# Kernel optimization log

Measured on AMD Instinct MI355X. Metric: run time of the kernel, lower is better.

The kernel has to match this reference:

```python
import jax, jax.numpy as jnp
import numpy as np

TOKENS = 8192       # batch 4 * seq 2048
D_IN = 4096
D_OUT = 4096


def setup_inputs() -> dict:
    key = jax.random.key(0)
    k_x, k_w, k_s, k_b = jax.random.split(key, 4)
    x = jax.random.normal(k_x, (TOKENS, D_IN), dtype=jnp.float32)
    # symmetric int8 quantized weight rows in [-128, 127]
    weight_q = jax.random.randint(k_w, (D_OUT, D_IN), -128, 128, dtype=jnp.int32)
    # per-output-channel scales (positive, small, like max_abs / 127)
    scales = jax.random.uniform(k_s, (D_OUT,), dtype=jnp.float32, minval=1e-4, maxval=2e-2)
    bias = jax.random.normal(k_b, (D_OUT,), dtype=jnp.float32)
    return {"x": x, "weight_q": weight_q, "scales": scales, "bias": bias}


def reference(x, weight_q, scales, bias):
    # Per-channel dequant: W[o, i] = weight_q[o, i] * scales[o]  (zero_point = 0)
    w = weight_q.astype(jnp.float32) * scales[:, None]          # [D_OUT, D_IN]
    # F.linear: x @ W^T + bias
    return jnp.einsum("ti,oi->to", x, w) + bias                 # [TOKENS, D_OUT]
```

## Files before the change

kernel.cpp:

```cpp
#include <hip/hip_runtime.h>
#include <stdint.h>

#define M_TOK 8192
#define N_OUT 4096
#define K_IN  4096

#define BM 256
#define BN 256
#define BK 128
#define NT (K_IN / BK)
#define NIT (NT / 2)

typedef __attribute__((ext_vector_type(4))) int i32x4;

__global__ void quant_x_kernel(const float* __restrict__ x,
                               char* __restrict__ A8,
                               float* __restrict__ sx) {
  int row = blockIdx.x * 4 + (threadIdx.x >> 6);
  int lane = threadIdx.x & 63;
  const float* xr = x + (size_t)row * K_IN;

  float4 v[4][4];
  float mx = 0.f;
#pragma unroll
  for (int c = 0; c < 4; ++c) {
    int base = c * 1024 + lane * 16;
#pragma unroll
    for (int j = 0; j < 4; ++j) {
      v[c][j] = *reinterpret_cast<const float4*>(xr + base + j * 4);
      mx = fmaxf(mx, fmaxf(fmaxf(fabsf(v[c][j].x), fabsf(v[c][j].y)),
                           fmaxf(fabsf(v[c][j].z), fabsf(v[c][j].w))));
    }
  }
#pragma unroll
  for (int m = 32; m > 0; m >>= 1) mx = fmaxf(mx, __shfl_xor(mx, m));

  float inv = (mx > 0.f) ? (127.0f / mx) : 0.f;
  if (lane == 0) sx[row] = (mx > 0.f) ? (mx / 127.0f) : 1.0f;

#pragma unroll
  for (int c = 0; c < 4; ++c) {
    int qi[16];
#pragma unroll
    for (int j = 0; j < 4; ++j) {
      qi[j * 4 + 0] = __float2int_rn(v[c][j].x * inv);
      qi[j * 4 + 1] = __float2int_rn(v[c][j].y * inv);
      qi[j * 4 + 2] = __float2int_rn(v[c][j].z * inv);
      qi[j * 4 + 3] = __float2int_rn(v[c][j].w * inv);
    }
    int4 p;
    int* pp = (int*)&p;
#pragma unroll
    for (int w = 0; w < 4; ++w) {
      int a0 = min(127, max(-127, qi[w * 4 + 0])) & 0xff;
      int a1 = min(127, max(-127, qi[w * 4 + 1])) & 0xff;
      int a2 = min(127, max(-127, qi[w * 4 + 2])) & 0xff;
      int a3 = min(127, max(-127, qi[w * 4 + 3])) & 0xff;
      pp[w] = a0 | (a1 << 8) | (a2 << 16) | (a3 << 24);
    }
    *reinterpret_cast<int4*>(A8 + (size_t)row * K_IN + c * 1024 + lane * 16) = p;
  }
}

__global__ void pack_w_kernel(const int* __restrict__ wq, char* __restrict__ B8) {
  const int total = (N_OUT * K_IN) / 16;
  for (int i = blockIdx.x * blockDim.x + threadIdx.x; i < total;
       i += gridDim.x * blockDim.x) {
    int4 p;
    int* pp = (int*)&p;
#pragma unroll
    for (int w = 0; w < 4; ++w) {
      int4 s = reinterpret_cast<const int4*>(wq)[i * 4 + w];
      pp[w] = (s.x & 0xff) | ((s.y & 0xff) << 8) | ((s.z & 0xff) << 16) |
              ((s.w & 0xff) << 24);
    }
    reinterpret_cast<int4*>(B8)[i] = p;
  }
}

#define GLOAD_LDS16(gptr, lptr)                                               \
  __builtin_amdgcn_global_load_lds(                                           \
      (const __attribute__((address_space(1))) void*)(gptr),                  \
      (__attribute__((address_space(3))) void*)(lptr), 16, 0, 0)

#define WAITCNT(s) asm volatile("s_waitcnt " s ::: "memory")

#define LDSA(buf, mh, fm, kk)                                                 \
  (*reinterpret_cast<const i32x4*>(                                           \
      lds + (buf)*65536 + (mh)*16384 + aRow + (fm)*2048 +                     \
      (((((kk)*4) | sBase) ^ sXor) << 4)))
#define LDSB(buf, nh, fn, kk)                                                 \
  (*reinterpret_cast<const i32x4*>(                                           \
      lds + (buf)*65536 + 32768 + (nh)*16384 + bRow + (fn)*2048 +             \
      (((((kk)*4) | sBase) ^ sXor) << 4)))

#define STAGE_A(buf, h, kt)                                                   \
  do {                                                                        \
    const char* _s = stA + (size_t)(h) * 128 * K_IN + (kt) * BK;              \
    GLOAD_LDS16(_s, lds + (buf)*65536 + (h)*16384 + ldsW0);                   \
    GLOAD_LDS16(_s + (size_t)64 * K_IN,                                       \
                lds + (buf)*65536 + (h)*16384 + 8192 + ldsW0);                \
  } while (0)
#define STAGE_B(buf, h, kt)                                                   \
  do {                                                                        \
    const char* _s = stB + (size_t)(h) * 128 * K_IN + (kt) * BK;              \
    GLOAD_LDS16(_s, lds + (buf)*65536 + 32768 + (h)*16384 + ldsW0);           \
    GLOAD_LDS16(_s + (size_t)64 * K_IN,                                       \
                lds + (buf)*65536 + 32768 + (h)*16384 + 8192 + ldsW0);        \
  } while (0)

#define MFMA16(mh, nh, BR)                                                    \
  do {                                                                        \
    _Pragma("unroll") for (int fm = 0; fm < 4; ++fm)                          \
    _Pragma("unroll") for (int fn = 0; fn < 2; ++fn) {                        \
      acc[mh][nh][fm][fn] = __builtin_amdgcn_mfma_i32_16x16x64_i8(            \
          aR[fm][0], BR[fn][0], acc[mh][nh][fm][fn], 0, 0, 0);                \
      acc[mh][nh][fm][fn] = __builtin_amdgcn_mfma_i32_16x16x64_i8(            \
          aR[fm][1], BR[fn][1], acc[mh][nh][fm][fn], 0, 0, 0);                \
    }                                                                         \
  } while (0)

#define PH_MID()                                                              \
  __builtin_amdgcn_s_barrier();                                               \
  WAITCNT("lgkmcnt(0)");                                                      \
  __builtin_amdgcn_sched_barrier(0);                                          \
  __builtin_amdgcn_s_setprio(1)

#define PH_END()                                                              \
  __builtin_amdgcn_s_setprio(0);                                              \
  __builtin_amdgcn_s_barrier();                                               \
  __builtin_amdgcn_sched_barrier(0)

#define PH_END_VM()                                                           \
  __builtin_amdgcn_s_setprio(0);                                              \
  WAITCNT("vmcnt(6)");                                                        \
  __builtin_amdgcn_sched_barrier(0);                                          \
  __builtin_amdgcn_s_barrier();                                               \
  __builtin_amdgcn_sched_barrier(0)

__global__ __launch_bounds__(512, 2) void gemm_8ph_i8(
    const char* __restrict__ A,
    const char* __restrict__ B,
    const float* __restrict__ sx,
    const float* __restrict__ scales,
    const float* __restrict__ bias,
    float* __restrict__ out) {
  __shared__ __align__(1024) char lds[131072];

  int bid = blockIdx.x;
  int swz = (bid & 7) * (512 / 8) + (bid >> 3);
  int bx = swz & 15;
  int by = swz >> 4;

  int tid = threadIdx.x;
  int lane = tid & 63;
  int wid = tid >> 6;
  int wm = wid >> 2;
  int wn = wid & 3;

  int aRow = (wm * 64 + (lane & 15)) * 128;
  int bRow = (wn * 32 + (lane & 15)) * 128;
  int sBase = lane >> 4;
  int sXor = lane & 7;

  const char* stA = A + (size_t)(by * BM + wid * 8 + (lane >> 3)) * K_IN +
                    ((lane & 7) ^ (lane >> 3)) * 16;
  const char* stB = B + (size_t)(bx * BN + wid * 8 + (lane >> 3)) * K_IN +
                    ((lane & 7) ^ (lane >> 3)) * 16;
  int ldsW0 = wid * 1024;

  i32x4 acc[2][2][4][2] = {};
  i32x4 aR[4][2];
  i32x4 bR0[2][2], bR1[2][2];

  STAGE_A(0, 0, 0); STAGE_A(0, 1, 0); STAGE_B(0, 0, 0); STAGE_B(0, 1, 0);
  WAITCNT("vmcnt(4)");
  STAGE_A(1, 0, 1); STAGE_B(1, 0, 1); STAGE_B(1, 1, 1);
  WAITCNT("vmcnt(6)");
  __builtin_amdgcn_s_barrier();
  __builtin_amdgcn_sched_barrier(0);

#pragma unroll 1
  for (int it = 0; it < NIT; ++it) {
    int kt1 = 2 * it + 1;
    int kt2 = (2 * it + 2) & (NT - 1);
    int kt3 = (2 * it + 3) & (NT - 1);

#pragma unroll
    for (int fm = 0; fm < 4; ++fm) { aR[fm][0] = LDSA(0, 0, fm, 0); aR[fm][1] = LDSA(0, 0, fm, 1); }
#pragma unroll
    for (int fn = 0; fn < 2; ++fn) { bR0[fn][0] = LDSB(0, 0, fn, 0); bR0[fn][1] = LDSB(0, 0, fn, 1); }
    STAGE_A(1, 1, kt1);
    WAITCNT("lgkmcnt(8)");
    PH_MID();
    MFMA16(0, 0, bR0);
    PH_END();

#pragma unroll
    for (int fn = 0; fn < 2; ++fn) { bR1[fn][0] = LDSB(0, 1, fn, 0); bR1[fn][1] = LDSB(0, 1, fn, 1); }
    STAGE_A(0, 0, kt2);
    PH_MID();
    MFMA16(0, 1, bR1);
    PH_END();

#pragma unroll
    for (int fm = 0; fm < 4; ++fm) { aR[fm][0] = LDSA(0, 1, fm, 0); aR[fm][1] = LDSA(0, 1, fm, 1); }
    STAGE_B(0, 0, kt2);
    PH_MID();
    MFMA16(1, 1, bR1);
    PH_END();

    STAGE_B(0, 1, kt2);
    PH_MID();
    MFMA16(1, 0, bR0);
    PH_END_VM();

#pragma unroll
    for (int fm = 0; fm < 4; ++fm) { aR[fm][0] = LDSA(1, 0, fm, 0); aR[fm][1] = LDSA(1, 0, fm, 1); }
#pragma unroll
    for (int fn = 0; fn < 2; ++fn) { bR0[fn][0] = LDSB(1, 0, fn, 0); bR0[fn][1] = LDSB(1, 0, fn, 1); }
    STAGE_A(0, 1, kt2);
    WAITCNT("lgkmcnt(8)");
    PH_MID();
    MFMA16(0, 0, bR0);
    PH_END();

#pragma unroll
    for (int fn = 0; fn < 2; ++fn) { bR1[fn][0] = LDSB(1, 1, fn, 0); bR1[fn][1] = LDSB(1, 1, fn, 1); }
    STAGE_A(1, 0, kt3);
    PH_MID();
    MFMA16(0, 1, bR1);
    PH_END();

#pragma unroll
    for (int fm = 0; fm < 4; ++fm) { aR[fm][0] = LDSA(1, 1, fm, 0); aR[fm][1] = LDSA(1, 1, fm, 1); }
    STAGE_B(1, 0, kt3);
    PH_MID();
    MFMA16(1, 1, bR1);
    PH_END();

    STAGE_B(1, 1, kt3);
    PH_MID();
    MFMA16(1, 0, bR0);
    PH_END_VM();
  }

  float sxv[2][4][4];
#pragma unroll
  for (int mh = 0; mh < 2; ++mh)
#pragma unroll
    for (int fm = 0; fm < 4; ++fm) {
      int row0 = by * BM + mh * 128 + wm * 64 + fm * 16 + (lane >> 4) * 4;
#pragma unroll
      for (int r = 0; r < 4; ++r) sxv[mh][fm][r] = sx[row0 + r];
    }

#pragma unroll
  for (int nh = 0; nh < 2; ++nh)
#pragma unroll
    for (int fn = 0; fn < 2; ++fn) {
      int col = bx * BN + nh * 128 + wn * 32 + fn * 16 + (lane & 15);
      float so = scales[col];
      float bv = bias[col];
#pragma unroll
      for (int mh = 0; mh < 2; ++mh)
#pragma unroll
        for (int fm = 0; fm < 4; ++fm) {
          int row0 = by * BM + mh * 128 + wm * 64 + fm * 16 + (lane >> 4) * 4;
          i32x4 v = acc[mh][nh][fm][fn];
#pragma unroll
          for (int r = 0; r < 4; ++r)
            out[(size_t)(row0 + r) * N_OUT + col] =
                (float)v[r] * (sxv[mh][fm][r] * so) + bv;
        }
    }
}

__global__ void fallback_gemm(const float* __restrict__ x,
                              const int* __restrict__ wq,
                              const float* __restrict__ scales,
                              const float* __restrict__ bias,
                              float* __restrict__ out) {
  __shared__ float xs[64][33];
  __shared__ float ws_[64][33];
  int tx = threadIdx.x & 15;
  int ty = threadIdx.x >> 4;
  int brow = blockIdx.y * 64, bcol = blockIdx.x * 64;
  float acc[4][4] = {};
  for (int k0 = 0; k0 < K_IN; k0 += 32) {
    for (int i = threadIdx.x; i < 64 * 32; i += 256) {
      int r = i >> 5, c = i & 31;
      xs[r][c] = x[(size_t)(brow + r) * K_IN + k0 + c];
      ws_[r][c] = (float)wq[(size_t)(bcol + r) * K_IN + k0 + c];
    }
    __syncthreads();
#pragma unroll 8
    for (int k = 0; k < 32; ++k) {
      float xv[4], wv[4];
#pragma unroll
      for (int i = 0; i < 4; ++i) xv[i] = xs[ty * 4 + i][k];
#pragma unroll
      for (int j = 0; j < 4; ++j) wv[j] = ws_[tx * 4 + j][k];
#pragma unroll
      for (int i = 0; i < 4; ++i)
#pragma unroll
        for (int j = 0; j < 4; ++j) acc[i][j] += xv[i] * wv[j];
    }
    __syncthreads();
  }
#pragma unroll
  for (int i = 0; i < 4; ++i)
#pragma unroll
    for (int j = 0; j < 4; ++j) {
      int o = bcol + tx * 4 + j;
      out[(size_t)(brow + ty * 4 + i) * N_OUT + o] = acc[i][j] * scales[o] + bias[o];
    }
}

extern "C" void kernel_launch(void* const* d_in, const int* in_sizes, int n_in,
                              void* d_out, int out_size, void* d_ws, size_t ws_size,
                              hipStream_t stream) {
  const float* x = (const float*)d_in[0];
  const int* wq = (const int*)d_in[1];
  const float* scales = (const float*)d_in[2];
  const float* bias = (const float*)d_in[3];
  float* out = (float*)d_out;

  const size_t offB = (size_t)M_TOK * K_IN;
  const size_t offS = offB + (size_t)N_OUT * K_IN;
  const size_t need = offS + (size_t)M_TOK * 4;

  if (ws_size >= need) {
    char* A8 = (char*)d_ws;
    char* B8 = (char*)d_ws + offB;
    float* sx = (float*)((char*)d_ws + offS);
    quant_x_kernel<<<M_TOK / 4, 256, 0, stream>>>(x, A8, sx);
    pack_w_kernel<<<2048, 256, 0, stream>>>(wq, B8);
    gemm_8ph_i8<<<(M_TOK / BM) * (N_OUT / BN), 512, 0, stream>>>(
        A8, B8, sx, scales, bias, out);
  } else {
    dim3 grid(N_OUT / 64, M_TOK / 64);
    fallback_gemm<<<grid, 256, 0, stream>>>(x, wq, scales, bias, out);
  }
}
```

Measured before the change: 187.6 us.

## Switch GEMM to 32x32x32 int8 MFMA and merge prep kernels into one launch

Replaces the 16x16x64 int8 MFMA tiling with 32x32x32 int8 MFMA, which changes the LDS fragment addressing, the accumulator layout (i32x16) and the epilogue row mapping. It also fuses the activation quantization and weight packing kernels into a single launch using block-index dispatch. The larger MFMA shape is meant to cut LDS read traffic per flop and the instruction count, and the merged prep removes one kernel launch. The trade-off is higher register pressure from the wider accumulators and a different per-instruction throughput profile.

New measurement: 198.0 us. 5.6% more time.

```diff
diff --git a/kernel.cpp b/kernel.cpp
--- a/kernel.cpp
+++ b/kernel.cpp
@@ -12,69 +12,72 @@
 #define NIT (NT / 2)
 
 typedef __attribute__((ext_vector_type(4))) int i32x4;
-
-__global__ void quant_x_kernel(const float* __restrict__ x,
-                               char* __restrict__ A8,
-                               float* __restrict__ sx) {
-  int row = blockIdx.x * 4 + (threadIdx.x >> 6);
-  int lane = threadIdx.x & 63;
-  const float* xr = x + (size_t)row * K_IN;
-
-  float4 v[4][4];
-  float mx = 0.f;
-#pragma unroll
-  for (int c = 0; c < 4; ++c) {
-    int base = c * 1024 + lane * 16;
-#pragma unroll
-    for (int j = 0; j < 4; ++j) {
-      v[c][j] = *reinterpret_cast<const float4*>(xr + base + j * 4);
-      mx = fmaxf(mx, fmaxf(fmaxf(fabsf(v[c][j].x), fabsf(v[c][j].y)),
-                           fmaxf(fabsf(v[c][j].z), fabsf(v[c][j].w))));
-    }
-  }
-#pragma unroll
-  for (int m = 32; m > 0; m >>= 1) mx = fmaxf(mx, __shfl_xor(mx, m));
-
-  float inv = (mx > 0.f) ? (127.0f / mx) : 0.f;
-  if (lane == 0) sx[row] = (mx > 0.f) ? (mx / 127.0f) : 1.0f;
-
-#pragma unroll
-  for (int c = 0; c < 4; ++c) {
-    int qi[16];
-#pragma unroll
-    for (int j = 0; j < 4; ++j) {
-      qi[j * 4 + 0] = __float2int_rn(v[c][j].x * inv);
-      qi[j * 4 + 1] = __float2int_rn(v[c][j].y * inv);
-      qi[j * 4 + 2] = __float2int_rn(v[c][j].z * inv);
-      qi[j * 4 + 3] = __float2int_rn(v[c][j].w * inv);
-    }
-    int4 p;
-    int* pp = (int*)&p;
-#pragma unroll
-    for (int w = 0; w < 4; ++w) {
-      int a0 = min(127, max(-127, qi[w * 4 + 0])) & 0xff;
-      int a1 = min(127, max(-127, qi[w * 4 + 1])) & 0xff;
-      int a2 = min(127, max(-127, qi[w * 4 + 2])) & 0xff;
-      int a3 = min(127, max(-127, qi[w * 4 + 3])) & 0xff;
-      pp[w] = a0 | (a1 << 8) | (a2 << 16) | (a3 << 24);
-    }
-    *reinterpret_cast<int4*>(A8 + (size_t)row * K_IN + c * 1024 + lane * 16) = p;
-  }
-}
-
-__global__ void pack_w_kernel(const int* __restrict__ wq, char* __restrict__ B8) {
-  const int total = (N_OUT * K_IN) / 16;
-  for (int i = blockIdx.x * blockDim.x + threadIdx.x; i < total;
-       i += gridDim.x * blockDim.x) {
-    int4 p;
-    int* pp = (int*)&p;
-#pragma unroll
-    for (int w = 0; w < 4; ++w) {
-      int4 s = reinterpret_cast<const int4*>(wq)[i * 4 + w];
-      pp[w] = (s.x & 0xff) | ((s.y & 0xff) << 8) | ((s.z & 0xff) << 16) |
-              ((s.w & 0xff) << 24);
-    }
-    reinterpret_cast<int4*>(B8)[i] = p;
+typedef __attribute__((ext_vector_type(16))) int i32x16;
+
+__global__ void prep_kernel(const float* __restrict__ x,
+                            const int* __restrict__ wq,
+                            char* __restrict__ A8,
+                            float* __restrict__ sx,
+                            char* __restrict__ B8) {
+  if (blockIdx.x < M_TOK / 4) {
+    int row = blockIdx.x * 4 + (threadIdx.x >> 6);
+    int lane = threadIdx.x & 63;
+    const float* xr = x + (size_t)row * K_IN;
+
+    float4 v[4][4];
+    float mx = 0.f;
+#pragma unroll
+    for (int c = 0; c < 4; ++c) {
+      int base = c * 1024 + lane * 16;
+#pragma unroll
+      for (int j = 0; j < 4; ++j) {
+        v[c][j] = *reinterpret_cast<const float4*>(xr + base + j * 4);
+        mx = fmaxf(mx, fmaxf(fmaxf(fabsf(v[c][j].x), fabsf(v[c][j].y)),
+                             fmaxf(fabsf(v[c][j].z), fabsf(v[c][j].w))));
+      }
+    }
+#pragma unroll
+    for (int m = 32; m > 0; m >>= 1) mx = fmaxf(mx, __shfl_xor(mx, m));
+
+    float inv = (mx > 0.f) ? (127.0f / mx) : 0.f;
+    if (lane == 0) sx[row] = (mx > 0.f) ? (mx / 127.0f) : 1.0f;
+
+#pragma unroll
+    for (int c = 0; c < 4; ++c) {
+      int qi[16];
+#pragma unroll
+      for (int j = 0; j < 4; ++j) {
+        qi[j * 4 + 0] = __float2int_rn(v[c][j].x * inv);
+        qi[j * 4 + 1] = __float2int_rn(v[c][j].y * inv);
+        qi[j * 4 + 2] = __float2int_rn(v[c][j].z * inv);
+        qi[j * 4 + 3] = __float2int_rn(v[c][j].w * inv);
+      }
+      int4 p;
+      int* pp = (int*)&p;
+#pragma unroll
+      for (int w = 0; w < 4; ++w) {
+        int a0 = min(127, max(-127, qi[w * 4 + 0])) & 0xff;
+        int a1 = min(127, max(-127, qi[w * 4 + 1])) & 0xff;
+        int a2 = min(127, max(-127, qi[w * 4 + 2])) & 0xff;
+        int a3 = min(127, max(-127, qi[w * 4 + 3])) & 0xff;
+        pp[w] = a0 | (a1 << 8) | (a2 << 16) | (a3 << 24);
+      }
+      *reinterpret_cast<int4*>(A8 + (size_t)row * K_IN + c * 1024 + lane * 16) = p;
+    }
+  } else {
+    const int total = (N_OUT * K_IN) / 16;
+    int idx = (blockIdx.x - M_TOK / 4) * blockDim.x + threadIdx.x;
+    for (int i = idx; i < total; i += 1024 * 256) {
+      int4 p;
+      int* pp = (int*)&p;
+#pragma unroll
+      for (int w = 0; w < 4; ++w) {
+        int4 s = reinterpret_cast<const int4*>(wq)[i * 4 + w];
+        pp[w] = (s.x & 0xff) | ((s.y & 0xff) << 8) | ((s.z & 0xff) << 16) |
+                ((s.w & 0xff) << 24);
+      }
+      reinterpret_cast<int4*>(B8)[i] = p;
+    }
   }
 }
 
@@ -85,14 +88,14 @@
 
 #define WAITCNT(s) asm volatile("s_waitcnt " s ::: "memory")
 
-#define LDSA(buf, mh, fm, kk)                                                 \
+#define LDSA32(buf, mh, t, ks)                                                \
   (*reinterpret_cast<const i32x4*>(                                           \
-      lds + (buf)*65536 + (mh)*16384 + aRow + (fm)*2048 +                     \
-      (((((kk)*4) | sBase) ^ sXor) << 4)))
-#define LDSB(buf, nh, fn, kk)                                                 \
+      lds + (buf)*65536 + (mh)*16384 + (t)*4096 + aRowB +                     \
+      (((((ks)*2) | sHi) ^ sXor) << 4)))
+#define LDSB32(buf, nh, ks)                                                   \
   (*reinterpret_cast<const i32x4*>(                                           \
-      lds + (buf)*65536 + 32768 + (nh)*16384 + bRow + (fn)*2048 +             \
-      (((((kk)*4) | sBase) ^ sXor) << 4)))
+      lds + (buf)*65536 + 32768 + (nh)*16384 + bRowB +                        \
+      (((((ks)*2) | sHi) ^ sXor) << 4)))
 
 #define STAGE_A(buf, h, kt)                                                   \
   do {                                                                        \
@@ -109,15 +112,12 @@
                 lds + (buf)*65536 + 32768 + (h)*16384 + 8192 + ldsW0);        \
   } while (0)
 
-#define MFMA16(mh, nh, BR)                                                    \
+#define MFMA8(mh, nh, BR)                                                     \
   do {                                                                        \
-    _Pragma("unroll") for (int fm = 0; fm < 4; ++fm)                          \
-    _Pragma("unroll") for (int fn = 0; fn < 2; ++fn) {                        \
-      acc[mh][nh][fm][fn] = __builtin_amdgcn_mfma_i32_16x16x64_i8(            \
-          aR[fm][0], BR[fn][0], acc[mh][nh][fm][fn], 0, 0, 0);                \
-      acc[mh][nh][fm][fn] = __builtin_amdgcn_mfma_i32_16x16x64_i8(            \
-          aR[fm][1], BR[fn][1], acc[mh][nh][fm][fn], 0, 0, 0);                \
-    }                                                                         \
+    _Pragma("unroll") for (int ks = 0; ks < 4; ++ks)                          \
+    _Pragma("unroll") for (int t = 0; t < 2; ++t)                             \
+      acc[2 * (mh) + t][nh] = __builtin_amdgcn_mfma_i32_32x32x32_i8(          \
+          aR[t][ks], BR[ks], acc[2 * (mh) + t][nh], 0, 0, 0);                 \
   } while (0)
 
 #define PH_MID()                                                              \
@@ -138,7 +138,7 @@
   __builtin_amdgcn_s_barrier();                                               \
   __builtin_amdgcn_sched_barrier(0)
 
-__global__ __launch_bounds__(512, 2) void gemm_8ph_i8(
+__global__ __launch_bounds__(512, 2) void gemm_8ph_i8w(
     const char* __restrict__ A,
     const char* __restrict__ B,
     const float* __restrict__ sx,
@@ -158,9 +158,9 @@
   int wm = wid >> 2;
   int wn = wid & 3;
 
-  int aRow = (wm * 64 + (lane & 15)) * 128;
-  int bRow = (wn * 32 + (lane & 15)) * 128;
-  int sBase = lane >> 4;
+  int aRowB = (wm * 64 + (lane & 31)) * 128;
+  int bRowB = (wn * 32 + (lane & 31)) * 128;
+  int sHi = lane >> 5;
   int sXor = lane & 7;
 
   const char* stA = A + (size_t)(by * BM + wid * 8 + (lane >> 3)) * K_IN +
@@ -169,9 +169,9 @@
                     ((lane & 7) ^ (lane >> 3)) * 16;
   int ldsW0 = wid * 1024;
 
-  i32x4 acc[2][2][4][2] = {};
-  i32x4 aR[4][2];
-  i32x4 bR0[2][2], bR1[2][2];
+  i32x16 acc[4][2] = {};
+  i32x4 aR[2][4];
+  i32x4 bR0[4], bR1[4];
 
   STAGE_A(0, 0, 0); STAGE_A(0, 1, 0); STAGE_B(0, 0, 0); STAGE_B(0, 1, 0);
   WAITCNT("vmcnt(4)");
@@ -187,93 +187,93 @@
     int kt3 = (2 * it + 3) & (NT - 1);
 
 #pragma unroll
-    for (int fm = 0; fm < 4; ++fm) { aR[fm][0] = LDSA(0, 0, fm, 0); aR[fm][1] = LDSA(0, 0, fm, 1); }
-#pragma unroll
-    for (int fn = 0; fn < 2; ++fn) { bR0[fn][0] = LDSB(0, 0, fn, 0); bR0[fn][1] = LDSB(0, 0, fn, 1); }
+    for (int t = 0; t < 2; ++t)
+#pragma unroll
+      for (int ks = 0; ks < 4; ++ks) aR[t][ks] = LDSA32(0, 0, t, ks);
+#pragma unroll
+    for (int ks = 0; ks < 4; ++ks) bR0[ks] = LDSB32(0, 0, ks);
     STAGE_A(1, 1, kt1);
     WAITCNT("lgkmcnt(8)");
     PH_MID();
-    MFMA16(0, 0, bR0);
-    PH_END();
-
-#pragma unroll
-    for (int fn = 0; fn < 2; ++fn) { bR1[fn][0] = LDSB(0, 1, fn, 0); bR1[fn][1] = LDSB(0, 1, fn, 1); }
+    MFMA8(0, 0, bR0);
+    PH_END();
+
+#pragma unroll
+    for (int ks = 0; ks < 4; ++ks) bR1[ks] = LDSB32(0, 1, ks);
     STAGE_A(0, 0, kt2);
     PH_MID();
-    MFMA16(0, 1, bR1);
-    PH_END();
-
-#pragma unroll
-    for (int fm = 0; fm < 4; ++fm) { aR[fm][0] = LDSA(0, 1, fm, 0); aR[fm][1] = LDSA(0, 1, fm, 1); }
+    MFMA8(0, 1, bR1);
+    PH_END();
+
+#pragma unroll
+    for (int t = 0; t < 2; ++t)
+#pragma unroll
+      for (int ks = 0; ks < 4; ++ks) aR[t][ks] = LDSA32(0, 1, t, ks);
     STAGE_B(0, 0, kt2);
     PH_MID();
-    MFMA16(1, 1, bR1);
+    MFMA8(1, 1, bR1);
     PH_END();
 
     STAGE_B(0, 1, kt2);
     PH_MID();
-    MFMA16(1, 0, bR0);
+    MFMA8(1, 0, bR0);
     PH_END_VM();
 
 #pragma unroll
-    for (int fm = 0; fm < 4; ++fm) { aR[fm][0] = LDSA(1, 0, fm, 0); aR[fm][1] = LDSA(1, 0, fm, 1); }
-#pragma unroll
-    for (int fn = 0; fn < 2; ++fn) { bR0[fn][0] = LDSB(1, 0, fn, 0); bR0[fn][1] = LDSB(1, 0, fn, 1); }
+    for (int t = 0; t < 2; ++t)
+#pragma unroll
+      for (int ks = 0; ks < 4; ++ks) aR[t][ks] = LDSA32(1, 0, t, ks);
+#pragma unroll
+    for (int ks = 0; ks < 4; ++ks) bR0[ks] = LDSB32(1, 0, ks);
     STAGE_A(0, 1, kt2);
     WAITCNT("lgkmcnt(8)");
     PH_MID();
-    MFMA16(0, 0, bR0);
-    PH_END();
-
-#pragma unroll
-    for (int fn = 0; fn < 2; ++fn) { bR1[fn][0] = LDSB(1, 1, fn, 0); bR1[fn][1] = LDSB(1, 1, fn, 1); }
+    MFMA8(0, 0, bR0);
+    PH_END();
+
+#pragma unroll
+    for (int ks = 0; ks < 4; ++ks) bR1[ks] = LDSB32(1, 1, ks);
     STAGE_A(1, 0, kt3);
     PH_MID();
-    MFMA16(0, 1, bR1);
-    PH_END();
-
-#pragma unroll
-    for (int fm = 0; fm < 4; ++fm) { aR[fm][0] = LDSA(1, 1, fm, 0); aR[fm][1] = LDSA(1, 1, fm, 1); }
+    MFMA8(0, 1, bR1);
+    PH_END();
+
+#pragma unroll
+    for (int t = 0; t < 2; ++t)
+#pragma unroll
+      for (int ks = 0; ks < 4; ++ks) aR[t][ks] = LDSA32(1, 1, t, ks);
     STAGE_B(1, 0, kt3);
     PH_MID();
-    MFMA16(1, 1, bR1);
+    MFMA8(1, 1, bR1);
     PH_END();
 
     STAGE_B(1, 1, kt3);
     PH_MID();
-    MFMA16(1, 0, bR0);
+    MFMA8(1, 0, bR0);
     PH_END_VM();
   }
 
-  float sxv[2][4][4];
-#pragma unroll
-  for (int mh = 0; mh < 2; ++mh)
-#pragma unroll
-    for (int fm = 0; fm < 4; ++fm) {
-      int row0 = by * BM + mh * 128 + wm * 64 + fm * 16 + (lane >> 4) * 4;
-#pragma unroll
-      for (int r = 0; r < 4; ++r) sxv[mh][fm][r] = sx[row0 + r];
-    }
-
-#pragma unroll
-  for (int nh = 0; nh < 2; ++nh)
-#pragma unroll
-    for (int fn = 0; fn < 2; ++fn) {
-      int col = bx * BN + nh * 128 + wn * 32 + fn * 16 + (lane & 15);
+#pragma unroll
+  for (int tm = 0; tm < 4; ++tm) {
+    int mh = tm >> 1, t = tm & 1;
+    int rbase = by * BM + mh * 128 + wm * 64 + t * 32 + 4 * sHi;
+    float sxr[16];
+#pragma unroll
+    for (int reg = 0; reg < 16; ++reg)
+      sxr[reg] = sx[rbase + (reg & 3) + 8 * (reg >> 2)];
+#pragma unroll
+    for (int nh = 0; nh < 2; ++nh) {
+      int col = bx * BN + nh * 128 + wn * 32 + (lane & 31);
       float so = scales[col];
       float bv = bias[col];
-#pragma unroll
-      for (int mh = 0; mh < 2; ++mh)
-#pragma unroll
-        for (int fm = 0; fm < 4; ++fm) {
-          int row0 = by * BM + mh * 128 + wm * 64 + fm * 16 + (lane >> 4) * 4;
-          i32x4 v = acc[mh][nh][fm][fn];
-#pragma unroll
-          for (int r = 0; r < 4; ++r)
-            out[(size_t)(row0 + r) * N_OUT + col] =
-                (float)v[r] * (sxv[mh][fm][r] * so) + bv;
-        }
-    }
+      i32x16 v = acc[tm][nh];
+#pragma unroll
+      for (int reg = 0; reg < 16; ++reg) {
+        int row = rbase + (reg & 3) + 8 * (reg >> 2);
+        out[(size_t)row * N_OUT + col] = (float)v[reg] * (sxr[reg] * so) + bv;
+      }
+    }
+  }
 }
 
 __global__ void fallback_gemm(const float* __restrict__ x,
@@ -334,9 +334,8 @@
     char* A8 = (char*)d_ws;
     char* B8 = (char*)d_ws + offB;
     float* sx = (float*)((char*)d_ws + offS);
-    quant_x_kernel<<<M_TOK / 4, 256, 0, stream>>>(x, A8, sx);
-    pack_w_kernel<<<2048, 256, 0, stream>>>(wq, B8);
-    gemm_8ph_i8<<<(M_TOK / BM) * (N_OUT / BN), 512, 0, stream>>>(
+    prep_kernel<<<M_TOK / 4 + 1024, 256, 0, stream>>>(x, wq, A8, sx, B8);
+    gemm_8ph_i8w<<<(M_TOK / BM) * (N_OUT / BN), 512, 0, stream>>>(
         A8, B8, sx, scales, bias, out);
   } else {
     dim3 grid(N_OUT / 64, M_TOK / 64);
```
